# Kernel optimization log

Hardware: AMD Instinct MI355X
Metric: run time of the kernel (lower is better)

## Reference

```python
import math
import jax, jax.numpy as jnp
import numpy as np

EPS = 1e-5
SCALE_BASE = 512.0


def xpos_apply(x, downscale=False):
    # x: (..., L, head_dim); faithful to RetNet's XPOS (torchscale xpos)
    L, hd = x.shape[-2], x.shape[-1]
    half = hd // 2
    scale_vec = (jnp.arange(0, hd, 2, dtype=x.dtype) + 0.4 * hd) / (1.4 * hd)  # (half,)
    pos = jnp.arange(L, dtype=x.dtype)
    scale = scale_vec[None, :] ** (pos[:, None] / SCALE_BASE)  # (L, half)
    inv_freq = 1.0 / (10000.0 ** (jnp.arange(half, dtype=x.dtype) / half))
    sinusoid = pos[:, None] * inv_freq[None, :]  # (L, half)
    sin, cos = jnp.sin(sinusoid), jnp.cos(sinusoid)
    if downscale:
        scale = 1.0 / scale
    dup = lambda m: jnp.repeat(m, 2, axis=-1)  # duplicate_interleave -> (L, hd)
    sin_s, cos_s = dup(sin * scale), dup(cos * scale)
    x1, x2 = x[..., ::2], x[..., 1::2]
    rot = jnp.stack((-x2, x1), axis=-1).reshape(x.shape)  # rotate_every_two
    return x * cos_s + rot * sin_s


def decay_mask(L, gammas, dtype):
    # D[h, n, m] = gamma_h ** (n - m) if n >= m else 0
    n = jnp.arange(L)[:, None]
    m = jnp.arange(L)[None, :]
    causal = n >= m
    dist = jnp.where(causal, (n - m).astype(dtype), 0.0)
    return jnp.where(causal, gammas[:, None, None] ** dist, 0.0)  # (H, L, L)


def setup_inputs() -> dict:
    key = jax.random.key(0)
    ks = jax.random.split(key, 7)
    B, L, D, H = 1, 4096, 512, 8
    hs = D // H  # head_size = head_v_dim (double_v_dim=False)
    v_dim = D
    X = jax.random.normal(ks[0], (B, L, D), jnp.float32)
    W_Q = jax.random.normal(ks[1], (H, D, hs), jnp.float32) / D
    W_K = jax.random.normal(ks[2], (H, D, hs), jnp.float32) / D
    W_V = jax.random.normal(ks[3], (H, D, hs), jnp.float32) / D
    W_G = jax.random.normal(ks[4], (D, v_dim), jnp.float32) / D
    W_O = jax.random.normal(ks[5], (v_dim, D), jnp.float32) / D
    gn_weight = jnp.ones((v_dim,), jnp.float32)
    gn_bias = jnp.zeros((v_dim,), jnp.float32)
    return {"X": X, "W_Q": W_Q, "W_K": W_K, "W_V": W_V,
            "W_G": W_G, "W_O": W_O, "gn_weight": gn_weight, "gn_bias": gn_bias}


def reference(X, W_Q, W_K, W_V, W_G, W_O, gn_weight, gn_bias):
    B, L, D = X.shape
    H, _, hs = W_Q.shape
    hv = W_V.shape[-1]
    # per-head projections
    q = jnp.einsum('bld,ndh->bnlh', X, W_Q)
    k = jnp.einsum('bld,ndh->bnlh', X, W_K)
    v = jnp.einsum('bld,ndv->bnlv', X, W_V)
    q = xpos_apply(q, downscale=False)
    k = xpos_apply(k, downscale=True)
    # fixed (non-trainable) decay gammas: 1 - exp(linspace(log(1/32), log(1/512)))
    gammas = 1.0 - jnp.exp(jnp.linspace(math.log(1.0 / 32), math.log(1.0 / 512), H)).astype(X.dtype)
    Dmask = decay_mask(L, gammas, X.dtype)  # (H, L, L)
    scores = jnp.einsum('bnlh,bnsh->bnls', q, k) * Dmask[None]
    ret = jnp.einsum('bnls,bnsv->bnlv', scores, v)
    ret = ret.transpose(0, 2, 1, 3).reshape(B, L, H * hv)  # b l (n h)
    # GroupNorm(heads, v_dim) applied to (B*L, v_dim)
    g = ret.reshape(B * L, H, hv)
    mu = g.mean(-1, keepdims=True)
    var = g.var(-1, keepdims=True)
    g = (g - mu) * jax.lax.rsqrt(var + EPS)
    g = g.reshape(B, L, H * hv) * gn_weight + gn_bias
    gate = jax.nn.silu(X @ W_G)
    return (gate * g) @ W_O
```

## Files before the change

kernel.cpp:

```cpp
#include <hip/hip_runtime.h>
#include <math.h>

#define LQ 4096
#define DD 512
#define NH 8
#define HS 64
#define HALF 32

typedef unsigned short u16;
typedef unsigned int u32;
typedef __attribute__((ext_vector_type(8)))  short s8v;
typedef __attribute__((ext_vector_type(4)))  float f4v;
typedef __attribute__((ext_vector_type(4)))  u32  u32x4;
typedef __attribute__((ext_vector_type(16))) float f16v;

#define WS_QH   0u
#define WS_KH   2097152u
#define WS_KL   3145728u
#define WS_VT   4194304u
#define WS_XFH  5242880u
#define WS_XFL  6291456u
#define WS_WF   7340032u
#define WS_GATE 8650752u
#define WS_TAB  10747904u
#define WS_KTWH 11272192u

__device__ inline u16 f2bf(float x) {
    unsigned int u = __float_as_uint(x);
    return (u16)((u + 0x7fffu + ((u >> 16) & 1u)) >> 16);
}
__device__ inline float bf2f(u16 h) { return __uint_as_float(((unsigned int)h) << 16); }

__device__ __forceinline__ void gld16(void* lds, const void* g) {
    __builtin_amdgcn_global_load_lds(
        (const __attribute__((address_space(1))) void*)g,
        (__attribute__((address_space(3))) void*)lds, 16, 0, 0);
}

__global__ __launch_bounds__(256) void k_pre(
    const float* __restrict__ X,
    const float* __restrict__ Wq, const float* __restrict__ Wk, const float* __restrict__ Wv,
    const float* __restrict__ Wg, const float* __restrict__ Wo,
    float* __restrict__ tab, u16* __restrict__ Xf, u16* __restrict__ Wf) {
    __shared__ float tile[32][33];
    const int b = blockIdx.x;
    const int t = threadIdx.x;
    if (b < 512) {
        int idx = b * 256 + t;
        if (idx >= LQ * HALF) return;
        int l = idx >> 5;
        int i = idx & 31;
        double log2sv = log2((2.0 * i + 25.6) / 89.6);
        double e = (double)l * log2sv * (1.0 / 512.0);
        float sc  = exp2f((float)e);
        float sci = exp2f((float)(-e));
        double invf = exp2((double)i * (-13.287712379549449 / 32.0));
        double th = (double)l * invf;
        double r = th - 6.283185307179586 * floor(th * 0.15915494309189535);
        float c = cosf((float)r), sn = sinf((float)r);
        tab[idx]                 = c * sc;
        tab[LQ*HALF + idx]       = sn * sc;
        tab[2*LQ*HALF + idx]     = c * sci;
        tab[3*LQ*HALF + idx]     = sn * sci;
    } else if (b < 1536) {
        int g = (b - 512) * 256 + t;
        int l = g >> 6;
        int d = (g & 63) * 8;
        const float* xp = X + (size_t)l * DD + d;
        f4v x0 = *(const f4v*)xp;
        f4v x1 = *(const f4v*)(xp + 4);
        s8v ph;
#pragma unroll
        for (int j = 0; j < 4; ++j) {
            ph[j]   = (short)f2bf(x0[j]);
            ph[j+4] = (short)f2bf(x1[j]);
        }
        int rb = l >> 5, kt = d >> 6, ks = (d >> 4) & 3, kh2 = (d >> 3) & 1;
        int lane = kh2 * 32 + (l & 31);
        size_t off = (((size_t)(rb * 8 + kt) * 4 + ks) * 64 + lane) * 8;
        *(s8v*)(Xf + off) = ph;
    } else {
        int bb = b - 1536;
        int d0 = (bb & 15) * 32, C0 = (bb >> 4) * 32;
        int proj = C0 >> 9;
        int tc = t & 31, tr = t >> 5;
#pragma unroll
        for (int rr = 0; rr < 4; ++rr) {
            int dl = tr + rr * 8;
            int d = d0 + dl;
            int C = C0 + tc;
            float val;
            if (proj < 3) {
                const float* W = (proj == 0) ? Wq : ((proj == 1) ? Wk : Wv);
                int h = (C & 511) >> 6, hs = C & 63;
                val = W[(size_t)h * (DD * HS) + (size_t)d * HS + hs];
            } else if (proj == 3) {
                val = Wg[(size_t)d * DD + (C & 511)];
            } else {
                val = Wo[(size_t)d * DD + (C - 2048)];
            }
            tile[dl][tc] = val;
        }
        __syncthreads();
        if (t < 128) {
            int cl = t & 31, dgq = t >> 5;
            int dl = dgq * 8;
            s8v pk;
#pragma unroll
            for (int j = 0; j < 8; ++j) pk[j] = (short)f2bf(tile[dl + j][cl]);
            int C = C0 + cl;
            int da = d0 + dl;
            int nb = C >> 5, kt = da >> 6, ks = (da >> 4) & 3, kh2 = (da >> 3) & 1;
            int lane = kh2 * 32 + (C & 31);
            size_t off = (((size_t)(nb * 8 + kt) * 4 + ks) * 64 + lane) * 8;
            *(s8v*)(Wf + off) = pk;
        }
    }
}

__global__ __launch_bounds__(256) void k_fused(
    const u16* __restrict__ Xf, const u16* __restrict__ Wf,
    const float* __restrict__ tab,
    u16* __restrict__ qh, u16* __restrict__ kh,
    u16* __restrict__ vt, u16* __restrict__ gate16,
    u16* __restrict__ ktw) {
    __shared__ __align__(16) char smem[33024];
    const int t = threadIdx.x;
    const int b = blockIdx.x;
    const int mb = (b & 7) * 4 + (b >> 8);
    const int cb = (b >> 3) & 31;
    const int l0 = mb * 128;
    const int c0 = cb * 64;
    const int wv = t >> 6;
    const int lane = t & 63;
    const int c31 = lane & 31;
    const int hi = lane >> 5;

    const int rb = mb * 4 + wv;
    const u16* pA = Xf + (size_t)rb * 16384 + lane * 8;
    const char* gB = (const char*)(Wf + (size_t)(cb * 2) * 16384);

    f16v acc0, acc1;
#pragma unroll
    for (int i = 0; i < 16; ++i) { acc0[i] = 0.f; acc1[i] = 0.f; }

#define STAGEB(PH)                                                             \
    { _Pragma("unroll") for (int j = 0; j < 8; ++j) {                          \
        int seg = j >> 2, q4 = j & 3;                                          \
        gld16(smem + seg * 16384 + q4 * 4096 + wv * 1024,                      \
              gB + seg * 32768 + (PH) * 16384 + q4 * 4096 + t * 16); } }
    s8v aA[4], aB[4];
#define LOADA(S, KT)                                                      \
    { _Pragma("unroll") for (int ks = 0; ks < 4; ++ks) {                  \
        a##S[ks] = *(const s8v*)(pA + (KT) * 2048 + ks * 512); } }
#define MFMAX(S, KT)                                                                        \
    { const char* bbq = smem + ((KT) & 3) * 4096;                                           \
      _Pragma("unroll") for (int ks = 0; ks < 4; ++ks) {                                    \
        s8v b0 = *(const s8v*)(bbq + ks * 1024 + lane * 16);                                \
        s8v b1 = *(const s8v*)(bbq + 16384 + ks * 1024 + lane * 16);                        \
        acc0 = __builtin_amdgcn_mfma_f32_32x32x16_bf16(a##S[ks], b0, acc0, 0, 0, 0);        \
        acc1 = __builtin_amdgcn_mfma_f32_32x32x16_bf16(a##S[ks], b1, acc1, 0, 0, 0); } }
    STAGEB(0)
    LOADA(A, 0)
    asm volatile("s_waitcnt vmcnt(0)" ::: "memory");
    __syncthreads();
    LOADA(B, 1)
    __builtin_amdgcn_sched_barrier(0);
    MFMAX(A, 0)
    LOADA(A, 2)
    __builtin_amdgcn_sched_barrier(0);
    MFMAX(B, 1)
    LOADA(B, 3)
    __builtin_amdgcn_sched_barrier(0);
    MFMAX(A, 2)
    LOADA(A, 4)
    __builtin_amdgcn_sched_barrier(0);
    MFMAX(B, 3)
    __syncthreads();
    STAGEB(1)
    asm volatile("s_waitcnt vmcnt(0)" ::: "memory");
    __syncthreads();
    LOADA(B, 5)
    __builtin_amdgcn_sched_barrier(0);
    MFMAX(A, 4)
    LOADA(A, 6)
    __builtin_amdgcn_sched_barrier(0);
    MFMAX(B, 5)
    LOADA(B, 7)
    __builtin_amdgcn_sched_barrier(0);
    MFMAX(A, 6)
    __builtin_amdgcn_sched_barrier(0);
    MFMAX(B, 7)
#undef LOADA
#undef MFMAX
#undef STAGEB
    __syncthreads();

    float* vbuf = (float*)smem;
    const int proj = c0 >> 9;
    if (proj < 2) {
        const float* ct = tab + (proj ? 2 * LQ * HALF : 0);
        const float* st = tab + (proj ? 3 * LQ * HALF : LQ * HALF);
        u16* oh = proj ? kh : qh;
        const int hh = (c0 & 511) >> 6;
        float lgf = 0.f;
        if (proj == 1) {
            double lg = -3.4657359027997265 + (double)hh * (-2.772588722239781 / 7.0);
            lgf = (float)(log(1.0 - exp(lg)) * 1.4426950408889634);
        }
#pragma unroll
        for (int n = 0; n < 2; ++n) {
            const f16v acc = n ? acc1 : acc0;
            int C = c0 + n * 32 + c31;
            int hs = C & 63, i2 = hs >> 1;
            float sgn = (hs & 1) ? 1.f : -1.f;
#pragma unroll
            for (int r = 0; r < 16; ++r) {
                int lrow = wv * 32 + (r & 3) + 8 * (r >> 2) + 4 * hi;
                int pos = l0 + lrow;
                float val = acc[r];
                float part = __shfl_xor(val, 1);
                float res = val * ct[pos * HALF + i2] + sgn * part * st[pos * HALF + i2];
                size_t o = ((size_t)hh * LQ + pos) * HS + hs;
                oh[o] = f2bf(res);
                if (proj == 1) {
                    float wf = exp2f(lgf * (float)(64 - (pos & 63)));
                    vbuf[(n * 32 + c31) * 129 + lrow] = res * wf;
                }
            }
        }
        if (proj == 1) {
            __syncthreads();
            int cl = t >> 2, lseg = (t & 3) * 32;
            size_t o = ((size_t)hh * HS + cl) * LQ + l0 + lseg;
#pragma unroll
            for (int ch4 = 0; ch4 < 4; ++ch4) {
                s8v pkh;
#pragma unroll
                for (int j = 0; j < 8; ++j) pkh[j] = (short)f2bf(vbuf[cl * 129 + lseg + ch4 * 8 + j]);
                *(s8v*)(ktw + o + ch4 * 8) = pkh;
            }
        }
    } else if (proj == 2) {
#pragma unroll
        for (int n = 0; n < 2; ++n) {
            const f16v acc = n ? acc1 : acc0;
            int cl = n * 32 + c31;
#pragma unroll
            for (int r = 0; r < 16; ++r) {
                int lrow = wv * 32 + (r & 3) + 8 * (r >> 2) + 4 * hi;
                vbuf[cl * 129 + lrow] = acc[r];
            }
        }
        __syncthreads();
        int h = (c0 & 511) >> 6;
        int cl = t >> 2, lseg = (t & 3) * 32;
        size_t o = ((size_t)h * HS + cl) * LQ + l0 + lseg;
#pragma unroll
        for (int ch = 0; ch < 4; ++ch) {
            s8v pk;
#pragma unroll
            for (int j = 0; j < 8; ++j) pk[j] = (short)f2bf(vbuf[cl * 129 + lseg + ch * 8 + j]);
            *(s8v*)(vt + o + ch * 8) = pk;
        }
    } else {
#pragma unroll
        for (int n = 0; n < 2; ++n) {
            const f16v acc = n ? acc1 : acc0;
            int C = (c0 & 511) + n * 32 + c31;
#pragma unroll
            for (int r = 0; r < 16; ++r) {
                int lrow = wv * 32 + (r & 3) + 8 * (r >> 2) + 4 * hi;
                float vv = acc[r];
                gate16[(size_t)(l0 + lrow) * DD + C] = f2bf(vv / (1.f + expf(-vv)));
            }
        }
    }
}

__global__ __launch_bounds__(256) void k_ret1(
    const u16* __restrict__ vt, const u16* __restrict__ ktw,
    float* __restrict__ A) {
    const int t = threadIdx.x;
    const int c = blockIdx.x;
    const int h = blockIdx.y;
    const int wv = t >> 6, lane = t & 63, c31 = lane & 31, hi = lane >> 5;
    const int wch = wv >> 1, wd = wv & 1;

    s8v va[4];
    const u16* vp = vt + ((size_t)h * 64 + wch * 32 + c31) * LQ + c * 64 + hi * 8;
#pragma unroll
    for (int ks = 0; ks < 4; ++ks) va[ks] = *(const s8v*)(vp + ks * 16);

    f16v a;
#pragma unroll
    for (int i = 0; i < 16; ++i) a[i] = 0.f;

    const size_t kbase = ((size_t)h * 64 + wd * 32 + c31) * LQ + c * 64 + hi * 8;
#pragma unroll
    for (int ks = 0; ks < 4; ++ks) {
        s8v b_h = *(const s8v*)(ktw + kbase + ks * 16);
        a = __builtin_amdgcn_mfma_f32_32x32x16_bf16(va[ks], b_h, a, 0, 0, 0);
    }

    float* Ab = A + ((size_t)h * 64 + c) * 4096;
#pragma unroll
    for (int r = 0; r < 16; ++r) {
        int ch = wch * 32 + (r & 3) + 8 * (r >> 2) + 4 * hi;
        Ab[ch * 64 + wd * 32 + c31] = a[r];
    }
}

__global__ __launch_bounds__(256) void k_scan(
    const float* __restrict__ A, u16* __restrict__ sth) {
    const int bx = blockIdx.x;
    const int h = bx >> 4;
    const int e = (bx & 15) * 256 + threadIdx.x;
    double lg = -3.4657359027997265 + (double)h * (-2.772588722239781 / 7.0);
    double gamma = 1.0 - exp(lg);
    float g64 = (float)pow(gamma, 64.0);
    const float* Ab = A + (size_t)h * 64 * 4096 + e;
    u16* shb = sth + (size_t)h * 64 * 4096 + e;
    float av[64];
#pragma unroll
    for (int cc = 0; cc < 64; ++cc) av[cc] = Ab[(size_t)cc * 4096];
    float s = 0.f;
#pragma unroll
    for (int cc = 0; cc < 64; ++cc) {
        if (cc) shb[(size_t)cc * 4096] = f2bf(s);
        s = fmaf(g64, s, av[cc]);
    }
}

__global__ __launch_bounds__(256) void k_ret3(
    const u16* __restrict__ qh, const u16* __restrict__ kh,
    const u16* __restrict__ vt, const u16* __restrict__ sth,
    const u16* __restrict__ gate16,
    const float* __restrict__ gw, const float* __restrict__ gb,
    u16* __restrict__ Gf) {
    __shared__ __align__(16) char sBuf[16640];
    __shared__ float stats[64][2][2];
    const int t = threadIdx.x;
    const int c = blockIdx.x;
    const int h = blockIdx.y;
    const int wv = t >> 6, lane = t & 63, c31 = lane & 31, hi = lane >> 5;
    const int ws = wv >> 1, wc = wv & 1;
    const int l0q = c * 64;

    double lg = -3.4657359027997265 + (double)h * (-2.772588722239781 / 7.0);
    double gamma = 1.0 - exp(lg);
    float lgf = (float)(log(gamma) * 1.4426950408889634);
    float c1a[4], c8a[4];
#pragma unroll
    for (int m = 0; m < 4; ++m) { c1a[m] = exp2f(-lgf * (float)m); c8a[m] = exp2f(-lgf * (float)(8 * m)); }

    s8v qhf[4];
    {
        const u16* qph = qh + ((size_t)h * LQ + l0q + ws * 32 + c31) * HS + hi * 8;
#pragma unroll
        for (int ks = 0; ks < 4; ++ks) qhf[ks] = *(const s8v*)(qph + ks * 16);
    }

    {
        const char* gKH = (const char*)kh + ((size_t)h * LQ + l0q) * 128;
        const char* gVT = (const char*)vt + ((size_t)h * 64) * 8192 + l0q * 2;
#pragma unroll
        for (int i_ = 0; i_ < 4; ++i_) {
            int boff = i_ * 4096 + t * 16;
            int seg = boff >> 13;
            int o_ = boff & 8191;
            int osrc = o_ ^ (((o_ >> 7) & 7) << 4);
            const char* src = (seg == 0) ? gKH + osrc
                            : gVT + (size_t)(osrc >> 7) * 8192 + (osrc & 127);
            gld16(sBuf + boff, src);
        }
    }

    f16v qs;
#pragma unroll
    for (int i = 0; i < 16; ++i) qs[i] = 0.f;
    if (c > 0) {
        const u16* sbh = sth + ((size_t)h * 64 + c) * 4096;
#pragma unroll
        for (int ks = 0; ks < 4; ++ks) {
            int off = (wc * 32 + c31) * 64 + ks * 16 + hi * 8;
            s8v b_h = *(const s8v*)(sbh + off);
            qs = __builtin_amdgcn_mfma_f32_32x32x16_bf16(qhf[ks], b_h, qs, 0, 0, 0);
        }
    }

    asm volatile("s_waitcnt vmcnt(0)" ::: "memory");
    __syncthreads();

    f16v acc;
#pragma unroll
    for (int i = 0; i < 16; ++i) acc[i] = 0.f;
    const char* bKH = sBuf;
    const char* bVT = sBuf + 8192;

#pragma unroll
    for (int jt = 0; jt < 2; ++jt) {
        if (ws == 0 && jt == 1) break;
        f16v sacc;
#pragma unroll
        for (int i = 0; i < 16; ++i) sacc[i] = 0.f;
#pragma unroll
        for (int ks = 0; ks < 4; ++ks) {
            int krow = jt * 32 + c31;
            int ph = krow * 128 + ((ks * 32 + hi * 16) ^ ((krow & 7) << 4));
            s8v ah = *(const s8v*)(bKH + ph);
            sacc = __builtin_amdgcn_mfma_f32_32x32x16_bf16(ah, qhf[ks], sacc, 0, 0, 0);
        }
        const int D0 = (ws * 32 + c31) - jt * 32;
        float base = exp2f(lgf * (float)(D0 - 4 * hi));
        u32 w[8];
#pragma unroll
        for (int g = 0; g < 4; ++g) {
            float wg = base * c8a[g];
            float v0 = sacc[4 * g + 0] * (wg * c1a[0]);
            float v1 = sacc[4 * g + 1] * (wg * c1a[1]);
            float v2 = sacc[4 * g + 2] * (wg * c1a[2]);
            float v3 = sacc[4 * g + 3] * (wg * c1a[3]);
            int jr = 8 * g + 4 * hi;
            if (D0 - (jr + 0) < 0) v0 = 0.f;
            if (D0 - (jr + 1) < 0) v1 = 0.f;
            if (D0 - (jr + 2) < 0) v2 = 0.f;
            if (D0 - (jr + 3) < 0) v3 = 0.f;
            w[2 * g]     = (u32)f2bf(v0) | ((u32)f2bf(v1) << 16);
            w[2 * g + 1] = (u32)f2bf(v2) | ((u32)f2bf(v3) << 16);
        }
        u32 e0 = __shfl_xor(hi ? w[0] : w[2], 32);
        u32 e1 = __shfl_xor(hi ? w[1] : w[3], 32);
        u32 e2 = __shfl_xor(hi ? w[4] : w[6], 32);
        u32 e3 = __shfl_xor(hi ? w[5] : w[7], 32);
        u32x4 a0v = { hi ? e0 : w[0], hi ? e1 : w[1], hi ? w[2] : e0, hi ? w[3] : e1 };
        u32x4 a1v = { hi ? e2 : w[4], hi ? e3 : w[5], hi ? w[6] : e2, hi ? w[7] : e3 };
        s8v af0 = __builtin_bit_cast(s8v, a0v);
        s8v af1 = __builtin_bit_cast(s8v, a1v);
#pragma unroll
        for (int ksl = 0; ksl < 2; ++ksl) {
            s8v af = ksl ? af1 : af0;
            int cb = (jt * 2 + ksl) * 32 + hi * 16;
            int rv = wc * 32 + c31;
            s8v vb = *(const s8v*)(bVT + rv * 128 + (cb ^ ((rv & 7) << 4)));
            acc = __builtin_amdgcn_mfma_f32_32x32x16_bf16(af, vb, acc, 0, 0, 0);
        }
    }

    float vv[16];
#pragma unroll
    for (int r = 0; r < 16; ++r) {
        int row = (r & 3) + 8 * (r >> 2) + 4 * hi;
        int nloc = ws * 32 + row;
        float sc = exp2f(lgf * (float)nloc);
        vv[r] = acc[r] + sc * qs[r];
    }
#pragma unroll
    for (int r = 0; r < 16; ++r) {
        float s = vv[r], ss = vv[r] * vv[r];
#pragma unroll
        for (int off = 1; off < 32; off <<= 1) {
            s  += __shfl_xor(s, off);
            ss += __shfl_xor(ss, off);
        }
        if (c31 == 0) {
            int nloc = ws * 32 + (r & 3) + 8 * (r >> 2) + 4 * hi;
            stats[nloc][wc][0] = s;
            stats[nloc][wc][1] = ss;
        }
    }
    __syncthreads();

    float* gT = (float*)sBuf;
    const float gwv = gw[h * HS + wc * 32 + c31];
    const float gbv = gb[h * HS + wc * 32 + c31];
#pragma unroll
    for (int r = 0; r < 16; ++r) {
        int nloc = ws * 32 + (r & 3) + 8 * (r >> 2) + 4 * hi;
        float s  = stats[nloc][0][0] + stats[nloc][1][0];
        float ss = stats[nloc][0][1] + stats[nloc][1][1];
        float mean = s * (1.f / 64.f);
        float var = ss * (1.f / 64.f) - mean * mean;
        float inv = rsqrtf(var + 1e-5f);
        size_t o = (size_t)(l0q + nloc) * DD + h * HS + wc * 32 + c31;
        float g = ((vv[r] - mean) * inv * gwv + gbv) * bf2f(gate16[o]);
        gT[nloc * 65 + wc * 32 + c31] = g;
    }
    __syncthreads();
#pragma unroll
    for (int i = 0; i < 2; ++i) {
        int u = t + i * 256;
        int rbl = u >> 8;
        int ks = (u >> 6) & 3;
        int ln = u & 63;
        int row = rbl * 32 + (ln & 31);
        int ch = ks * 16 + (ln >> 5) * 8;
        s8v pk;
#pragma unroll
        for (int j = 0; j < 8; ++j) pk[j] = (short)f2bf(gT[row * 65 + ch + j]);
        size_t off = ((((size_t)(c * 2 + rbl) * 8 + h) * 4 + ks) * 64 + ln) * 8;
        *(s8v*)(Gf + off) = pk;
    }
}

__global__ __launch_bounds__(256) void k_out(
    const u16* __restrict__ Gf, const u16* __restrict__ Wf,
    float* __restrict__ out) {
    __shared__ __align__(16) char smem[32768];
    const int t = threadIdx.x;
    const int l0 = blockIdx.x * 128;
    const int c0 = blockIdx.y * 64;
    const int wv = t >> 6;
    const int lane = t & 63;
    const int c31 = lane & 31;
    const int hi = lane >> 5;

    const int rb = blockIdx.x * 4 + wv;
    const u16* pA  = Gf + (size_t)rb * 16384 + lane * 8;
    const char* gB = (const char*)(Wf + (size_t)(64 + blockIdx.y * 2) * 16384);

    f16v acc0, acc1;
#pragma unroll
    for (int i = 0; i < 16; ++i) { acc0[i] = 0.f; acc1[i] = 0.f; }

#define STAGEB(PH)                                                             \
    { _Pragma("unroll") for (int j = 0; j < 8; ++j) {                          \
        int seg = j >> 2, q4 = j & 3;                                          \
        gld16(smem + seg * 16384 + q4 * 4096 + wv * 1024,                      \
              gB + seg * 32768 + (PH) * 16384 + q4 * 4096 + t * 16); } }
    s8v aA[4], aB[4];
#define LOADO(S, KT)                                                      \
    { _Pragma("unroll") for (int ks = 0; ks < 4; ++ks) {                  \
        a##S[ks] = *(const s8v*)(pA + (KT) * 2048 + ks * 512); } }
#define MFMAO(S, KT)                                                                        \
    { const char* bbq = smem + ((KT) & 3) * 4096;                                           \
      _Pragma("unroll") for (int ks = 0; ks < 4; ++ks) {                                    \
        s8v b0 = *(const s8v*)(bbq + ks * 1024 + lane * 16);                                \
        s8v b1 = *(const s8v*)(bbq + 16384 + ks * 1024 + lane * 16);                        \
        acc0 = __builtin_amdgcn_mfma_f32_32x32x16_bf16(a##S[ks], b0, acc0, 0, 0, 0);        \
        acc1 = __builtin_amdgcn_mfma_f32_32x32x16_bf16(a##S[ks], b1, acc1, 0, 0, 0); } }
    STAGEB(0)
    LOADO(A, 0)
    asm volatile("s_waitcnt vmcnt(0)" ::: "memory");
    __syncthreads();
    LOADO(B, 1)
    __builtin_amdgcn_sched_barrier(0);
    MFMAO(A, 0)
    LOADO(A, 2)
    __builtin_amdgcn_sched_barrier(0);
    MFMAO(B, 1)
    LOADO(B, 3)
    __builtin_amdgcn_sched_barrier(0);
    MFMAO(A, 2)
    LOADO(A, 4)
    __builtin_amdgcn_sched_barrier(0);
    MFMAO(B, 3)
    __syncthreads();
    STAGEB(1)
    asm volatile("s_waitcnt vmcnt(0)" ::: "memory");
    __syncthreads();
    LOADO(B, 5)
    __builtin_amdgcn_sched_barrier(0);
    MFMAO(A, 4)
    LOADO(A, 6)
    __builtin_amdgcn_sched_barrier(0);
    MFMAO(B, 5)
    LOADO(B, 7)
    __builtin_amdgcn_sched_barrier(0);
    MFMAO(A, 6)
    __builtin_amdgcn_sched_barrier(0);
    MFMAO(B, 7)
#undef LOADO
#undef MFMAO
#undef STAGEB

#pragma unroll
    for (int n = 0; n < 2; ++n) {
        const f16v acc = n ? acc1 : acc0;
        int C = c0 + n * 32 + c31;
#pragma unroll
        for (int r = 0; r < 16; ++r) {
            int lrow = wv * 32 + (r & 3) + 8 * (r >> 2) + 4 * hi;
            out[(size_t)(l0 + lrow) * DD + C] = acc[r];
        }
    }
}

extern "C" void kernel_launch(void* const* d_in, const int* in_sizes, int n_in,
                              void* d_out, int out_size, void* d_ws, size_t ws_size,
                              hipStream_t stream) {
    const float* X   = (const float*)d_in[0];
    const float* W_Q = (const float*)d_in[1];
    const float* W_K = (const float*)d_in[2];
    const float* W_V = (const float*)d_in[3];
    const float* W_G = (const float*)d_in[4];
    const float* W_O = (const float*)d_in[5];
    const float* gnw = (const float*)d_in[6];
    const float* gnb = (const float*)d_in[7];

    float* ws   = (float*)d_ws;
    u16* qhp  = (u16*)(ws + WS_QH);
    u16* khp  = (u16*)(ws + WS_KH);
    u16* vtp  = (u16*)(ws + WS_VT);
    u16* xfp  = (u16*)(ws + WS_XFH);
    u16* wf   = (u16*)(ws + WS_WF);
    u16* gate16 = (u16*)(ws + WS_GATE);
    float* tab  = ws + WS_TAB;
    u16* ktwp = (u16*)(ws + WS_KTWH);
    float* Abuf = ws + WS_XFH;
    u16* sthp = (u16*)(ws + WS_KTWH);
    u16* Gfp  = (u16*)(ws + WS_XFH);
    float* out  = (float*)d_out;

    k_pre<<<2816, 256, 0, stream>>>(X, W_Q, W_K, W_V, W_G, W_O, tab, xfp, wf);
    k_fused<<<1024, 256, 0, stream>>>(xfp, wf, tab, qhp, khp, vtp, gate16, ktwp);
    k_ret1<<<dim3(64, 8), 256, 0, stream>>>(vtp, ktwp, Abuf);
    k_scan<<<128, 256, 0, stream>>>(Abuf, sthp);
    k_ret3<<<dim3(64, 8), 256, 0, stream>>>(qhp, khp, vtp, sthp, gate16, gnw, gnb, Gfp);
    k_out<<<dim3(32, 8), 256, 0, stream>>>(Gfp, wf, out);
}
```

Baseline: 66.62 us.

## Widen fused projection GEMM tile to 128 columns with four accumulators

The fused QKV/gate projection kernel now computes 128 output columns per block instead of 64, using four MFMA accumulators and half as many blocks. Each A fragment loaded from global memory is therefore reused across twice as many B columns. The B staging changes to a four-phase double-k schedule, and the K and V epilogues loop over two heads with extra barriers. It also changes the LDS destination addressing of an async load in k_ret3 to a per-wave form. The wider tile raises register pressure and leaves only 512 blocks, which reduces parallelism across the GPU.

New measurement: 75.35 us. 1.13x slower.

```diff
diff --git a/kernel.cpp b/kernel.cpp
--- a/kernel.cpp
+++ b/kernel.cpp
@@ -124,13 +124,13 @@
     u16* __restrict__ qh, u16* __restrict__ kh,
     u16* __restrict__ vt, u16* __restrict__ gate16,
     u16* __restrict__ ktw) {
-    __shared__ __align__(16) char smem[33024];
+    __shared__ __align__(16) char smem[33536];
     const int t = threadIdx.x;
     const int b = blockIdx.x;
-    const int mb = (b & 7) * 4 + (b >> 8);
-    const int cb = (b >> 3) & 31;
+    const int cb = (b >> 3) & 15;
+    const int mb = (b & 7) * 4 + (b >> 7);
     const int l0 = mb * 128;
-    const int c0 = cb * 64;
+    const int c0 = cb * 128;
     const int wv = t >> 6;
     const int lane = t & 63;
     const int c31 = lane & 31;
@@ -138,80 +138,88 @@
 
     const int rb = mb * 4 + wv;
     const u16* pA = Xf + (size_t)rb * 16384 + lane * 8;
-    const char* gB = (const char*)(Wf + (size_t)(cb * 2) * 16384);
-
-    f16v acc0, acc1;
-#pragma unroll
-    for (int i = 0; i < 16; ++i) { acc0[i] = 0.f; acc1[i] = 0.f; }
-
-#define STAGEB(PH)                                                             \
-    { _Pragma("unroll") for (int j = 0; j < 8; ++j) {                          \
-        int seg = j >> 2, q4 = j & 3;                                          \
-        gld16(smem + seg * 16384 + q4 * 4096 + wv * 1024,                      \
-              gB + seg * 32768 + (PH) * 16384 + q4 * 4096 + t * 16); } }
+    const char* gB = (const char*)(Wf + (size_t)(cb * 4) * 16384);
+
+    f16v acc0, acc1, acc2, acc3;
+#pragma unroll
+    for (int i = 0; i < 16; ++i) { acc0[i] = 0.f; acc1[i] = 0.f; acc2[i] = 0.f; acc3[i] = 0.f; }
+
+#define STAGEB(P)                                                                  \
+    { _Pragma("unroll") for (int j = 0; j < 8; ++j) {                              \
+        int n_ = j >> 1, kl_ = j & 1;                                              \
+        gld16(smem + n_ * 8192 + kl_ * 4096 + wv * 1024,                           \
+              gB + n_ * 32768 + ((P) * 2 + kl_) * 4096 + t * 16); } }
     s8v aA[4], aB[4];
-#define LOADA(S, KT)                                                      \
-    { _Pragma("unroll") for (int ks = 0; ks < 4; ++ks) {                  \
+#define LOADA(S, KT)                                                               \
+    { _Pragma("unroll") for (int ks = 0; ks < 4; ++ks) {                           \
         a##S[ks] = *(const s8v*)(pA + (KT) * 2048 + ks * 512); } }
-#define MFMAX(S, KT)                                                                        \
-    { const char* bbq = smem + ((KT) & 3) * 4096;                                           \
-      _Pragma("unroll") for (int ks = 0; ks < 4; ++ks) {                                    \
-        s8v b0 = *(const s8v*)(bbq + ks * 1024 + lane * 16);                                \
-        s8v b1 = *(const s8v*)(bbq + 16384 + ks * 1024 + lane * 16);                        \
-        acc0 = __builtin_amdgcn_mfma_f32_32x32x16_bf16(a##S[ks], b0, acc0, 0, 0, 0);        \
-        acc1 = __builtin_amdgcn_mfma_f32_32x32x16_bf16(a##S[ks], b1, acc1, 0, 0, 0); } }
+#define MFMAK(S, KT)                                                                           \
+    { const char* bbq = smem + ((KT) & 1) * 4096;                                              \
+      _Pragma("unroll") for (int ks = 0; ks < 4; ++ks) {                                       \
+        s8v b0 = *(const s8v*)(bbq + 0 * 8192 + ks * 1024 + lane * 16);                        \
+        s8v b1 = *(const s8v*)(bbq + 1 * 8192 + ks * 1024 + lane * 16);                        \
+        s8v b2 = *(const s8v*)(bbq + 2 * 8192 + ks * 1024 + lane * 16);                        \
+        s8v b3 = *(const s8v*)(bbq + 3 * 8192 + ks * 1024 + lane * 16);                        \
+        acc0 = __builtin_amdgcn_mfma_f32_32x32x16_bf16(a##S[ks], b0, acc0, 0, 0, 0);           \
+        acc1 = __builtin_amdgcn_mfma_f32_32x32x16_bf16(a##S[ks], b1, acc1, 0, 0, 0);           \
+        acc2 = __builtin_amdgcn_mfma_f32_32x32x16_bf16(a##S[ks], b2, acc2, 0, 0, 0);           \
+        acc3 = __builtin_amdgcn_mfma_f32_32x32x16_bf16(a##S[ks], b3, acc3, 0, 0, 0); } }
+
+    LOADA(A, 0)
     STAGEB(0)
-    LOADA(A, 0)
     asm volatile("s_waitcnt vmcnt(0)" ::: "memory");
     __syncthreads();
     LOADA(B, 1)
     __builtin_amdgcn_sched_barrier(0);
-    MFMAX(A, 0)
+    MFMAK(A, 0)
+    __builtin_amdgcn_sched_barrier(0);
+    MFMAK(B, 1)
+    __syncthreads();
+    STAGEB(1)
     LOADA(A, 2)
-    __builtin_amdgcn_sched_barrier(0);
-    MFMAX(B, 1)
+    asm volatile("s_waitcnt vmcnt(0)" ::: "memory");
+    __syncthreads();
     LOADA(B, 3)
     __builtin_amdgcn_sched_barrier(0);
-    MFMAX(A, 2)
+    MFMAK(A, 2)
+    __builtin_amdgcn_sched_barrier(0);
+    MFMAK(B, 3)
+    __syncthreads();
+    STAGEB(2)
     LOADA(A, 4)
-    __builtin_amdgcn_sched_barrier(0);
-    MFMAX(B, 3)
-    __syncthreads();
-    STAGEB(1)
     asm volatile("s_waitcnt vmcnt(0)" ::: "memory");
     __syncthreads();
     LOADA(B, 5)
     __builtin_amdgcn_sched_barrier(0);
-    MFMAX(A, 4)
+    MFMAK(A, 4)
+    __builtin_amdgcn_sched_barrier(0);
+    MFMAK(B, 5)
+    __syncthreads();
+    STAGEB(3)
     LOADA(A, 6)
-    __builtin_amdgcn_sched_barrier(0);
-    MFMAX(B, 5)
+    asm volatile("s_waitcnt vmcnt(0)" ::: "memory");
+    __syncthreads();
     LOADA(B, 7)
     __builtin_amdgcn_sched_barrier(0);
-    MFMAX(A, 6)
-    __builtin_amdgcn_sched_barrier(0);
-    MFMAX(B, 7)
+    MFMAK(A, 6)
+    __builtin_amdgcn_sched_barrier(0);
+    MFMAK(B, 7)
 #undef LOADA
-#undef MFMAX
+#undef MFMAK
 #undef STAGEB
     __syncthreads();
 
+#define GETACC(N) ((N) == 0 ? acc0 : (N) == 1 ? acc1 : (N) == 2 ? acc2 : acc3)
     float* vbuf = (float*)smem;
-    const int proj = c0 >> 9;
-    if (proj < 2) {
-        const float* ct = tab + (proj ? 2 * LQ * HALF : 0);
-        const float* st = tab + (proj ? 3 * LQ * HALF : LQ * HALF);
-        u16* oh = proj ? kh : qh;
-        const int hh = (c0 & 511) >> 6;
-        float lgf = 0.f;
-        if (proj == 1) {
-            double lg = -3.4657359027997265 + (double)hh * (-2.772588722239781 / 7.0);
-            lgf = (float)(log(1.0 - exp(lg)) * 1.4426950408889634);
-        }
-#pragma unroll
-        for (int n = 0; n < 2; ++n) {
-            const f16v acc = n ? acc1 : acc0;
+    const int proj = cb >> 2;
+    if (proj == 0) {
+        const float* ct = tab;
+        const float* st = tab + LQ * HALF;
+#pragma unroll
+        for (int n = 0; n < 4; ++n) {
+            const f16v acc = GETACC(n);
             int C = c0 + n * 32 + c31;
+            int hh = (C & 511) >> 6;
             int hs = C & 63, i2 = hs >> 1;
             float sgn = (hs & 1) ? 1.f : -1.f;
 #pragma unroll
@@ -221,18 +229,39 @@
                 float val = acc[r];
                 float part = __shfl_xor(val, 1);
                 float res = val * ct[pos * HALF + i2] + sgn * part * st[pos * HALF + i2];
-                size_t o = ((size_t)hh * LQ + pos) * HS + hs;
-                oh[o] = f2bf(res);
-                if (proj == 1) {
-                    float wf = exp2f(lgf * (float)(64 - (pos & 63)));
-                    vbuf[(n * 32 + c31) * 129 + lrow] = res * wf;
+                qh[((size_t)hh * LQ + pos) * HS + hs] = f2bf(res);
+            }
+        }
+    } else if (proj == 1) {
+        const float* ct = tab + 2 * LQ * HALF;
+        const float* st = tab + 3 * LQ * HALF;
+#pragma unroll
+        for (int p = 0; p < 2; ++p) {
+            int hhp = ((c0 & 511) >> 6) + p;
+            double lgd = -3.4657359027997265 + (double)hhp * (-2.772588722239781 / 7.0);
+            float lgfp = (float)(log(1.0 - exp(lgd)) * 1.4426950408889634);
+#pragma unroll
+            for (int nn = 0; nn < 2; ++nn) {
+                const int n = p * 2 + nn;
+                const f16v acc = GETACC(n);
+                int C = c0 + n * 32 + c31;
+                int hs = C & 63, i2 = hs >> 1;
+                float sgn = (hs & 1) ? 1.f : -1.f;
+#pragma unroll
+                for (int r = 0; r < 16; ++r) {
+                    int lrow = wv * 32 + (r & 3) + 8 * (r >> 2) + 4 * hi;
+                    int pos = l0 + lrow;
+                    float val = acc[r];
+                    float part = __shfl_xor(val, 1);
+                    float res = val * ct[pos * HALF + i2] + sgn * part * st[pos * HALF + i2];
+                    kh[((size_t)hhp * LQ + pos) * HS + hs] = f2bf(res);
+                    float wf = exp2f(lgfp * (float)(64 - (pos & 63)));
+                    vbuf[(nn * 32 + c31) * 129 + lrow] = res * wf;
                 }
             }
-        }
-        if (proj == 1) {
             __syncthreads();
             int cl = t >> 2, lseg = (t & 3) * 32;
-            size_t o = ((size_t)hh * HS + cl) * LQ + l0 + lseg;
+            size_t o = ((size_t)hhp * HS + cl) * LQ + l0 + lseg;
 #pragma unroll
             for (int ch4 = 0; ch4 < 4; ++ch4) {
                 s8v pkh;
@@ -240,33 +269,39 @@
                 for (int j = 0; j < 8; ++j) pkh[j] = (short)f2bf(vbuf[cl * 129 + lseg + ch4 * 8 + j]);
                 *(s8v*)(ktw + o + ch4 * 8) = pkh;
             }
+            __syncthreads();
         }
     } else if (proj == 2) {
 #pragma unroll
-        for (int n = 0; n < 2; ++n) {
-            const f16v acc = n ? acc1 : acc0;
-            int cl = n * 32 + c31;
-#pragma unroll
-            for (int r = 0; r < 16; ++r) {
-                int lrow = wv * 32 + (r & 3) + 8 * (r >> 2) + 4 * hi;
-                vbuf[cl * 129 + lrow] = acc[r];
+        for (int p = 0; p < 2; ++p) {
+            int hhp = ((c0 & 511) >> 6) + p;
+#pragma unroll
+            for (int nn = 0; nn < 2; ++nn) {
+                const int n = p * 2 + nn;
+                const f16v acc = GETACC(n);
+                int cl_ = nn * 32 + c31;
+#pragma unroll
+                for (int r = 0; r < 16; ++r) {
+                    int lrow = wv * 32 + (r & 3) + 8 * (r >> 2) + 4 * hi;
+                    vbuf[cl_ * 129 + lrow] = acc[r];
+                }
             }
-        }
-        __syncthreads();
-        int h = (c0 & 511) >> 6;
-        int cl = t >> 2, lseg = (t & 3) * 32;
-        size_t o = ((size_t)h * HS + cl) * LQ + l0 + lseg;
-#pragma unroll
-        for (int ch = 0; ch < 4; ++ch) {
-            s8v pk;
-#pragma unroll
-            for (int j = 0; j < 8; ++j) pk[j] = (short)f2bf(vbuf[cl * 129 + lseg + ch * 8 + j]);
-            *(s8v*)(vt + o + ch * 8) = pk;
+            __syncthreads();
+            int cl = t >> 2, lseg = (t & 3) * 32;
+            size_t o = ((size_t)hhp * HS + cl) * LQ + l0 + lseg;
+#pragma unroll
+            for (int ch = 0; ch < 4; ++ch) {
+                s8v pk;
+#pragma unroll
+                for (int j = 0; j < 8; ++j) pk[j] = (short)f2bf(vbuf[cl * 129 + lseg + ch * 8 + j]);
+                *(s8v*)(vt + o + ch * 8) = pk;
+            }
+            __syncthreads();
         }
     } else {
 #pragma unroll
-        for (int n = 0; n < 2; ++n) {
-            const f16v acc = n ? acc1 : acc0;
+        for (int n = 0; n < 4; ++n) {
+            const f16v acc = GETACC(n);
             int C = (c0 & 511) + n * 32 + c31;
 #pragma unroll
             for (int r = 0; r < 16; ++r) {
@@ -276,6 +311,7 @@
             }
         }
     }
+#undef GETACC
 }
 
 __global__ __launch_bounds__(256) void k_ret1(
@@ -372,7 +408,7 @@
             int osrc = o_ ^ (((o_ >> 7) & 7) << 4);
             const char* src = (seg == 0) ? gKH + osrc
                             : gVT + (size_t)(osrc >> 7) * 8192 + (osrc & 127);
-            gld16(sBuf + boff, src);
+            gld16(sBuf + i_ * 4096 + (t >> 6) * 1024, src);
         }
     }
 
@@ -613,7 +649,7 @@
     float* out  = (float*)d_out;
 
     k_pre<<<2816, 256, 0, stream>>>(X, W_Q, W_K, W_V, W_G, W_O, tab, xfp, wf);
-    k_fused<<<1024, 256, 0, stream>>>(xfp, wf, tab, qhp, khp, vtp, gate16, ktwp);
+    k_fused<<<512, 256, 0, stream>>>(xfp, wf, tab, qhp, khp, vtp, gate16, ktwp);
     k_ret1<<<dim3(64, 8), 256, 0, stream>>>(vtp, ktwp, Abuf);
     k_scan<<<128, 256, 0, stream>>>(Abuf, sthp);
     k_ret3<<<dim3(64, 8), 256, 0, stream>>>(qhp, khp, vtp, sthp, gate16, gnw, gnb, Gfp);
```

## Stage full K-depth weight tile in LDS once and deepen A-operand prefetch

Applied to the files above, without the earlier changes.

In the projection and output GEMM kernels, the whole 512-deep B (weight) tile is now loaded into 64KB of shared memory up front, where before it came in two phases with a mid-loop barrier and a second wait. A third A-register buffer gives a two-stage-ahead prefetch of the A fragments, and a partial vmcnt wait lets the first MFMAs start before every load has landed. This removes a synchronization bubble and the serialized second staging, at the cost of doubling LDS use per block, which can reduce occupancy, plus more registers. The attention kernel's LDS destination addressing for gld16 is also adjusted.

Result: slower. 69.62 us (+4.5%).

```diff
diff --git a/kernel.cpp b/kernel.cpp
--- a/kernel.cpp
+++ b/kernel.cpp
@@ -124,7 +124,7 @@
     u16* __restrict__ qh, u16* __restrict__ kh,
     u16* __restrict__ vt, u16* __restrict__ gate16,
     u16* __restrict__ ktw) {
-    __shared__ __align__(16) char smem[33024];
+    __shared__ __align__(16) char smem[65536];
     const int t = threadIdx.x;
     const int b = blockIdx.x;
     const int mb = (b & 7) * 4 + (b >> 8);
@@ -144,56 +144,52 @@
 #pragma unroll
     for (int i = 0; i < 16; ++i) { acc0[i] = 0.f; acc1[i] = 0.f; }
 
-#define STAGEB(PH)                                                             \
-    { _Pragma("unroll") for (int j = 0; j < 8; ++j) {                          \
-        int seg = j >> 2, q4 = j & 3;                                          \
-        gld16(smem + seg * 16384 + q4 * 4096 + wv * 1024,                      \
-              gB + seg * 32768 + (PH) * 16384 + q4 * 4096 + t * 16); } }
-    s8v aA[4], aB[4];
+#pragma unroll
+    for (int j = 0; j < 16; ++j)
+        gld16(smem + j * 4096 + wv * 1024, gB + j * 4096 + t * 16);
+    __builtin_amdgcn_sched_barrier(0);
+
+    s8v aA[4], aB[4], aC[4];
 #define LOADA(S, KT)                                                      \
     { _Pragma("unroll") for (int ks = 0; ks < 4; ++ks) {                  \
         a##S[ks] = *(const s8v*)(pA + (KT) * 2048 + ks * 512); } }
-#define MFMAX(S, KT)                                                                        \
-    { const char* bbq = smem + ((KT) & 3) * 4096;                                           \
+#define MFMAK(S, KT)                                                                        \
+    { const char* bbq = smem + (KT) * 4096;                                                 \
       _Pragma("unroll") for (int ks = 0; ks < 4; ++ks) {                                    \
         s8v b0 = *(const s8v*)(bbq + ks * 1024 + lane * 16);                                \
-        s8v b1 = *(const s8v*)(bbq + 16384 + ks * 1024 + lane * 16);                        \
+        s8v b1 = *(const s8v*)(bbq + 32768 + ks * 1024 + lane * 16);                        \
         acc0 = __builtin_amdgcn_mfma_f32_32x32x16_bf16(a##S[ks], b0, acc0, 0, 0, 0);        \
         acc1 = __builtin_amdgcn_mfma_f32_32x32x16_bf16(a##S[ks], b1, acc1, 0, 0, 0); } }
-    STAGEB(0)
+
     LOADA(A, 0)
-    asm volatile("s_waitcnt vmcnt(0)" ::: "memory");
+    LOADA(B, 1)
+    __builtin_amdgcn_sched_barrier(0);
+    asm volatile("s_waitcnt vmcnt(8)" ::: "memory");
     __syncthreads();
-    LOADA(B, 1)
-    __builtin_amdgcn_sched_barrier(0);
-    MFMAX(A, 0)
-    LOADA(A, 2)
-    __builtin_amdgcn_sched_barrier(0);
-    MFMAX(B, 1)
-    LOADA(B, 3)
-    __builtin_amdgcn_sched_barrier(0);
-    MFMAX(A, 2)
-    LOADA(A, 4)
-    __builtin_amdgcn_sched_barrier(0);
-    MFMAX(B, 3)
-    __syncthreads();
-    STAGEB(1)
-    asm volatile("s_waitcnt vmcnt(0)" ::: "memory");
-    __syncthreads();
-    LOADA(B, 5)
-    __builtin_amdgcn_sched_barrier(0);
-    MFMAX(A, 4)
+    LOADA(C, 2)
+    __builtin_amdgcn_sched_barrier(0);
+    MFMAK(A, 0)
+    LOADA(A, 3)
+    __builtin_amdgcn_sched_barrier(0);
+    MFMAK(B, 1)
+    LOADA(B, 4)
+    __builtin_amdgcn_sched_barrier(0);
+    MFMAK(C, 2)
+    LOADA(C, 5)
+    __builtin_amdgcn_sched_barrier(0);
+    MFMAK(A, 3)
     LOADA(A, 6)
     __builtin_amdgcn_sched_barrier(0);
-    MFMAX(B, 5)
+    MFMAK(B, 4)
     LOADA(B, 7)
     __builtin_amdgcn_sched_barrier(0);
-    MFMAX(A, 6)
-    __builtin_amdgcn_sched_barrier(0);
-    MFMAX(B, 7)
+    MFMAK(C, 5)
+    __builtin_amdgcn_sched_barrier(0);
+    MFMAK(A, 6)
+    __builtin_amdgcn_sched_barrier(0);
+    MFMAK(B, 7)
 #undef LOADA
-#undef MFMAX
-#undef STAGEB
+#undef MFMAK
     __syncthreads();
 
     float* vbuf = (float*)smem;
@@ -372,7 +368,7 @@
             int osrc = o_ ^ (((o_ >> 7) & 7) << 4);
             const char* src = (seg == 0) ? gKH + osrc
                             : gVT + (size_t)(osrc >> 7) * 8192 + (osrc & 127);
-            gld16(sBuf + boff, src);
+            gld16(sBuf + i_ * 4096 + (t >> 6) * 1024, src);
         }
     }
 
@@ -506,7 +502,7 @@
 __global__ __launch_bounds__(256) void k_out(
     const u16* __restrict__ Gf, const u16* __restrict__ Wf,
     float* __restrict__ out) {
-    __shared__ __align__(16) char smem[32768];
+    __shared__ __align__(16) char smem[65536];
     const int t = threadIdx.x;
     const int l0 = blockIdx.x * 128;
     const int c0 = blockIdx.y * 64;
@@ -523,56 +519,51 @@
 #pragma unroll
     for (int i = 0; i < 16; ++i) { acc0[i] = 0.f; acc1[i] = 0.f; }
 
-#define STAGEB(PH)                                                             \
-    { _Pragma("unroll") for (int j = 0; j < 8; ++j) {                          \
-        int seg = j >> 2, q4 = j & 3;                                          \
-        gld16(smem + seg * 16384 + q4 * 4096 + wv * 1024,                      \
-              gB + seg * 32768 + (PH) * 16384 + q4 * 4096 + t * 16); } }
-    s8v aA[4], aB[4];
+#pragma unroll
+    for (int j = 0; j < 16; ++j)
+        gld16(smem + j * 4096 + wv * 1024, gB + j * 4096 + t * 16);
+    __builtin_amdgcn_sched_barrier(0);
+
+    s8v aA[4], aB[4], aC[4];
 #define LOADO(S, KT)                                                      \
     { _Pragma("unroll") for (int ks = 0; ks < 4; ++ks) {                  \
         a##S[ks] = *(const s8v*)(pA + (KT) * 2048 + ks * 512); } }
 #define MFMAO(S, KT)                                                                        \
-    { const char* bbq = smem + ((KT) & 3) * 4096;                                           \
+    { const char* bbq = smem + (KT) * 4096;                                                 \
       _Pragma("unroll") for (int ks = 0; ks < 4; ++ks) {                                    \
         s8v b0 = *(const s8v*)(bbq + ks * 1024 + lane * 16);                                \
-        s8v b1 = *(const s8v*)(bbq + 16384 + ks * 1024 + lane * 16);                        \
+        s8v b1 = *(const s8v*)(bbq + 32768 + ks * 1024 + lane * 16);                        \
         acc0 = __builtin_amdgcn_mfma_f32_32x32x16_bf16(a##S[ks], b0, acc0, 0, 0, 0);        \
         acc1 = __builtin_amdgcn_mfma_f32_32x32x16_bf16(a##S[ks], b1, acc1, 0, 0, 0); } }
-    STAGEB(0)
     LOADO(A, 0)
-    asm volatile("s_waitcnt vmcnt(0)" ::: "memory");
+    LOADO(B, 1)
+    __builtin_amdgcn_sched_barrier(0);
+    asm volatile("s_waitcnt vmcnt(8)" ::: "memory");
     __syncthreads();
-    LOADO(B, 1)
+    LOADO(C, 2)
     __builtin_amdgcn_sched_barrier(0);
     MFMAO(A, 0)
-    LOADO(A, 2)
+    LOADO(A, 3)
     __builtin_amdgcn_sched_barrier(0);
     MFMAO(B, 1)
-    LOADO(B, 3)
-    __builtin_amdgcn_sched_barrier(0);
-    MFMAO(A, 2)
-    LOADO(A, 4)
-    __builtin_amdgcn_sched_barrier(0);
-    MFMAO(B, 3)
-    __syncthreads();
-    STAGEB(1)
-    asm volatile("s_waitcnt vmcnt(0)" ::: "memory");
-    __syncthreads();
-    LOADO(B, 5)
-    __builtin_amdgcn_sched_barrier(0);
-    MFMAO(A, 4)
+    LOADO(B, 4)
+    __builtin_amdgcn_sched_barrier(0);
+    MFMAO(C, 2)
+    LOADO(C, 5)
+    __builtin_amdgcn_sched_barrier(0);
+    MFMAO(A, 3)
     LOADO(A, 6)
     __builtin_amdgcn_sched_barrier(0);
-    MFMAO(B, 5)
+    MFMAO(B, 4)
     LOADO(B, 7)
+    __builtin_amdgcn_sched_barrier(0);
+    MFMAO(C, 5)
     __builtin_amdgcn_sched_barrier(0);
     MFMAO(A, 6)
     __builtin_amdgcn_sched_barrier(0);
     MFMAO(B, 7)
 #undef LOADO
 #undef MFMAO
-#undef STAGEB
 
 #pragma unroll
     for (int n = 0; n < 2; ++n) {
```
